# Optimization experiments

Hardware: AMD Instinct MI355X
Metric: run time of the kernel (lower is better)

## Reference

```python
import jax, jax.numpy as jnp
import numpy as np

B, S, DIM = 2, 2048, 4096
H, KVH = 32, 8
HD = DIM // H          # 128
N_REP = H // KVH       # 4
ROPE_THETA = 500000.0


def setup_inputs() -> dict:
    key = jax.random.key(0)
    ks = jax.random.split(key, 6)
    x = jax.random.normal(ks[0], (B, S, DIM), dtype=jnp.float32)
    sc = 1.0 / np.sqrt(DIM)
    wq = jax.random.normal(ks[1], (DIM, DIM), dtype=jnp.float32) * sc
    wk = jax.random.normal(ks[2], (KVH * HD, DIM), dtype=jnp.float32) * sc
    wv = jax.random.normal(ks[3], (KVH * HD, DIM), dtype=jnp.float32) * sc
    wo = jax.random.normal(ks[4], (DIM, DIM), dtype=jnp.float32) * sc
    # freqs_cis = exp(i * t * theta^{-2k/d}) -> cos/sin tables, shape (S, HD//2)
    inv_freq = 1.0 / (ROPE_THETA ** (np.arange(0, HD, 2, dtype=np.float32) / HD))
    t = np.arange(S, dtype=np.float32)
    angles = jnp.asarray(np.outer(t, inv_freq), dtype=jnp.float32)
    freqs_cos = jnp.cos(angles)
    freqs_sin = jnp.sin(angles)
    # causal additive mask (start_pos = 0 prefill)
    mask = jnp.triu(jnp.full((S, S), -1e9, dtype=jnp.float32), k=1)
    return {"x": x, "wq": wq, "wk": wk, "wv": wv, "wo": wo,
            "freqs_cos": freqs_cos, "freqs_sin": freqs_sin,
            "mask": mask, "start_pos": 0}


def _apply_rope(t, cos, sin):
    # t: [B,S,h,HD]; cos/sin: [S,HD//2] -> complex mult on pairs of last dim
    tr = t.reshape(*t.shape[:-1], HD // 2, 2)
    re, im = tr[..., 0], tr[..., 1]
    c = cos[None, :, None, :]
    s = sin[None, :, None, :]
    out_re = re * c - im * s
    out_im = re * s + im * c
    return jnp.stack([out_re, out_im], axis=-1).reshape(t.shape)


def reference(x, wq, wk, wv, wo, freqs_cos, freqs_sin, mask, start_pos):
    b, s, _ = x.shape
    xq = (x @ wq.T).reshape(b, s, H, HD)
    xk = (x @ wk.T).reshape(b, s, KVH, HD)
    xv = (x @ wv.T).reshape(b, s, KVH, HD)
    xq = _apply_rope(xq, freqs_cos, freqs_sin)
    xk = _apply_rope(xk, freqs_cos, freqs_sin)
    # start_pos == 0: KV cache slice [:, :start_pos+seqlen] == current xk/xv
    keys = jnp.repeat(xk, N_REP, axis=2)    # GQA expand -> [b,s,H,HD]
    values = jnp.repeat(xv, N_REP, axis=2)
    scores = jnp.einsum('bqhd,bkhd->bhqk', xq, keys) / jnp.sqrt(jnp.float32(HD))
    scores = scores + mask[None, None, :, :]
    probs = jax.nn.softmax(scores.astype(jnp.float32), axis=-1).astype(xq.dtype)
    out = jnp.einsum('bhqk,bkhd->bqhd', probs, values).reshape(b, s, H * HD)
    return out @ wo.T
```

## Files before the change

kernel.cpp:

```cpp
#include <hip/hip_runtime.h>


#define HN   32
#define KVHN 8
#define HDIM 128
#define SEQ  2048
#define NB   2
#define DIMM 4096
#define KVD  1024

typedef __attribute__((ext_vector_type(4))) float floatx4;
typedef __attribute__((ext_vector_type(8))) short bf16x8;
typedef unsigned short u16;
typedef unsigned int   u32;

__device__ __forceinline__ u16 f2bf(float f) {
  union { float f; u32 u; } x; x.f = f;
  u32 r = x.u + 0x7fffu + ((x.u >> 16) & 1u);
  return (u16)(r >> 16);
}

__device__ __forceinline__ void gload_lds16(const u16* g, u16* l) {
  __builtin_amdgcn_global_load_lds(
      (const __attribute__((address_space(1))) void*)g,
      (__attribute__((address_space(3))) void*)l, 16, 0, 0);
}

__global__ __launch_bounds__(256) void cast_f2bf_kernel(const float* __restrict__ in,
                                                        u16* __restrict__ out, int n) {
  int i = (blockIdx.x * 256 + threadIdx.x) * 8;
  if (i + 8 > n) return;
  const float4* p = (const float4*)(in + i);
  float4 a = p[0], b = p[1];
  union { u16 h[8]; uint4 v; } r;
  r.h[0] = f2bf(a.x); r.h[1] = f2bf(a.y); r.h[2] = f2bf(a.z); r.h[3] = f2bf(a.w);
  r.h[4] = f2bf(b.x); r.h[5] = f2bf(b.y); r.h[6] = f2bf(b.z); r.h[7] = f2bf(b.w);
  *(uint4*)(out + i) = r.v;
}


#define STG(tile, kind) do {                                                     \
    const int _t = (tile);                                                       \
    if (_t < NT) {                                                               \
      const int _kt = _t << 6;                                                   \
      u16* _buf = smem + ((_t & 1) << 15);                                       \
      const int _isB = (kind) & 1;                                               \
      const u16* _g = _isB ? Bb : Ab;                                            \
      u16* _lb = _isB ? _buf + 16384 : _buf;                                     \
      const int _hh = ((kind) >> 1);                                             \
      _Pragma("unroll")                                                          \
      for (int _cc = 0; _cc < 2; ++_cc) {                                        \
        const int _slot = _cc * 8 + w;                                           \
        const int _rb = _isB ? ((_slot >> 2) * 64 + _hh * 32 + (_slot & 3) * 8)  \
                             : ((_slot >> 3) * 128 + _hh * 64 + (_slot & 7) * 8);\
        const int _lrow = _rb + (l >> 3);                                        \
        const int _ck = (l & 7) ^ (l >> 3);                                      \
        gload_lds16(_g + (long)_lrow * K + _kt + _ck * 8,                        \
                    _lb + _rb * 64);                                             \
      }                                                                          \
    }                                                                            \
  } while (0)

#define LDA(bufAp, mh) do {                                                      \
    _Pragma("unroll") for (int mi = 0; mi < 4; ++mi)                             \
    _Pragma("unroll") for (int kk = 0; kk < 2; ++kk)                             \
      af[mi][kk] = *(const bf16x8*)&(bufAp)[                                     \
          (wm * 128 + (mh) * 64 + mi * 16 + c) * 64 + (((kk * 4 + g) ^ swz) * 8)]; \
  } while (0)

#define LDB(bufBp, nh) do {                                                      \
    _Pragma("unroll") for (int nj = 0; nj < 2; ++nj)                             \
    _Pragma("unroll") for (int kk = 0; kk < 2; ++kk)                             \
      bf[nh][nj][kk] = *(const bf16x8*)&(bufBp)[                                 \
          (wn * 64 + (nh) * 32 + nj * 16 + c) * 64 + (((kk * 4 + g) ^ swz) * 8)]; \
  } while (0)

#define MF16(mh, nh) do {                                                        \
    asm volatile("s_waitcnt lgkmcnt(0)");                                        \
    __builtin_amdgcn_s_setprio(1);                                               \
    _Pragma("unroll") for (int kk = 0; kk < 2; ++kk)                             \
    _Pragma("unroll") for (int mi = 0; mi < 4; ++mi)                             \
    _Pragma("unroll") for (int nj = 0; nj < 2; ++nj)                             \
      acc[mh][mi][nh][nj] = __builtin_amdgcn_mfma_f32_16x16x32_bf16(             \
          af[mi][kk], bf[nh][nj][kk], acc[mh][mi][nh][nj], 0, 0, 0);             \
    __builtin_amdgcn_s_setprio(0);                                               \
  } while (0)

#define BARF() do { asm volatile("" ::: "memory");                               \
                    __builtin_amdgcn_s_barrier();                                \
                    asm volatile("" ::: "memory"); } while (0)

#define HALF_ITER(curA, curB, s1t, s1k, s2t, s2k, s3t, s3k, s4t, s4k, LAST) do { \
    LDA(curA, 0); LDB(curB, 0); STG(s1t, s1k);                                   \
    BARF(); MF16(0, 0); BARF();                                                  \
    LDB(curB, 1); STG(s2t, s2k);                                                 \
    BARF(); MF16(0, 1); BARF();                                                  \
    LDA(curA, 1); STG(s3t, s3k);                                                 \
    BARF(); MF16(1, 0); BARF();                                                  \
    STG(s4t, s4k);                                                               \
    BARF(); MF16(1, 1);                                                          \
    if (LAST) { asm volatile("s_waitcnt vmcnt(0)" ::: "memory"); }               \
    else      { asm volatile("s_waitcnt vmcnt(6)" ::: "memory"); }               \
    BARF();                                                                      \
  } while (0)

template <int EPI>
__global__ __launch_bounds__(512, 2) void gemm256_nt(const u16* __restrict__ A, const u16* __restrict__ B,
                                                     void* __restrict__ Cv, void* __restrict__ Cv2,
                                                     int M, int N, int K,
                                                     const float* __restrict__ fc, const float* __restrict__ fs) {
  __shared__ u16 smem[65536];
  const int tid = threadIdx.x;
  const int w = tid >> 6, l = tid & 63, g = l >> 4, c = l & 15;
  const int wm = w >> 2, wn = w & 3;
  const int swz = c & 7;

  const int nwg = gridDim.x * gridDim.y;
  int lid = blockIdx.y * gridDim.x + blockIdx.x;
  lid = (lid & 7) * (nwg >> 3) + (lid >> 3);
  const int bx = lid % gridDim.x, by = lid / gridDim.x;
  const int m0 = by * 256, n0 = bx * 256;

  const u16* Ab = A + (long)m0 * K;
  const u16* Bb = B + (long)n0 * K;
  const int NT = K >> 6;
  const int NITER = NT >> 1;

  floatx4 acc[2][4][2][2] = {};
  bf16x8 af[4][2], bf[2][2][2];

  STG(0, 0); STG(0, 1); STG(0, 2); STG(0, 3);
  STG(1, 0); STG(1, 1); STG(1, 2);
  asm volatile("s_waitcnt vmcnt(6)" ::: "memory");
  BARF();

  const u16* A0p = smem;
  const u16* B0p = smem + 16384;
  const u16* A1p = smem + 32768;
  const u16* B1p = smem + 49152;

#pragma unroll 1
  for (int i = 0; i < NITER; ++i) {
    const bool last = (i == NITER - 1);
    const int t2 = 2 * i + 2, t3 = 2 * i + 3;
    HALF_ITER(A0p, B0p, 2 * i + 1, 3, t2, 0, t2, 1, t2, 2, last);
    HALF_ITER(A1p, B1p, t2, 3, t3, 0, t3, 1, t3, 2, last);
  }

#pragma unroll
  for (int mh = 0; mh < 2; ++mh)
#pragma unroll
  for (int mi = 0; mi < 4; ++mi)
#pragma unroll
  for (int nh = 0; nh < 2; ++nh)
#pragma unroll
  for (int nj = 0; nj < 2; ++nj) {
    const int colb = n0 + wn * 64 + nh * 32 + nj * 16;
    const int col = colb + c;
    const int rowb = m0 + wm * 128 + mh * 64 + mi * 16 + g * 4;
    floatx4 av = acc[mh][mi][nh][nj];
    if (EPI == 3 && colb >= 1024) {
      const int bb = rowb >> 11, s0 = rowb & (SEQ - 1);
      union { u16 h4[4]; uint2 v; } pk;
#pragma unroll
      for (int r = 0; r < 4; ++r) pk.h4[r] = f2bf(av[r]);
      *(uint2*)((u16*)Cv2 + ((long)(bb * 1024 + (col - 1024))) * SEQ + s0) = pk.v;
    } else {
#pragma unroll
      for (int r = 0; r < 4; ++r) {
        const int row = rowb + r;
        float v = av[r];
        if (EPI == 1 || EPI == 3) {
          float pv = __shfl_xor(v, 1);
          int pos = row & (SEQ - 1);
          int fi = (col & (HDIM - 1)) >> 1;
          float cs = fc[pos * (HDIM / 2) + fi];
          float sn = fs[pos * (HDIM / 2) + fi];
          v = (col & 1) ? (pv * sn + v * cs) : (v * cs - pv * sn);
          if (EPI == 1) v *= 0.08838834764831845f;
        }
        if (EPI == 2)      ((float*)Cv)[(long)row * N + col] = v;
        else if (EPI == 3) ((u16*)Cv)[(long)row * KVD + col] = f2bf(v);
        else               ((u16*)Cv)[(long)row * N + col] = f2bf(v);
      }
    }
  }
}

__global__ __launch_bounds__(256, 4) void flash_attn(const u16* __restrict__ q, const u16* __restrict__ kk,
                                                     const u16* __restrict__ vt, u16* __restrict__ o) {
  __shared__ u16 smem[20480];
  const int tid = threadIdx.x;
  const int w = tid >> 6, l = tid & 63, g = (l >> 4) & 3, c = l & 15;
  const int bh = blockIdx.y, b = bh >> 5, h = bh & 31, kvh = h >> 2;
  const int q0 = (31 - blockIdx.x) * 64;

  const u16* qg = q  + (long)(b * SEQ + q0) * DIMM + h * HDIM;
  const u16* kg = kk + (long)b * SEQ * KVD + kvh * HDIM;
  const u16* vg = vt + (long)(b * KVD + kvh * HDIM) * SEQ;

  const int r4 = l >> 4, ka16 = l & 15, r8 = l >> 3, ka8 = l & 7;

  {
#pragma unroll
    for (int cc = 0; cc < 4; ++cc) {
      int row = cc * 16 + w * 4 + r4;
      gload_lds16(qg + (long)row * DIMM + ((ka16 ^ (row & 7)) * 8), &smem[(cc * 16 + w * 4) * 128]);
    }
  }
  __syncthreads();
  bf16x8 qf[4];
#pragma unroll
  for (int t = 0; t < 4; ++t)
    qf[t] = *(const bf16x8*)&smem[(w * 16 + c) * 128 + ((t * 4 + g) ^ (c & 7)) * 8];
  __syncthreads();

  u16* sP = &smem[16384 + w * 1024];
  floatx4 oacc[8] = {};
  float mrow = -3e38f, lrow = 0.f;
  const int nkt = (q0 + 64) >> 6;
  const int qwave = q0 + w * 16;

#pragma unroll
  for (int cc = 0; cc < 4; ++cc) {
    int srow = cc * 16 + w * 4 + r4;
    gload_lds16(kg + (long)srow * KVD + ((ka16 ^ (srow & 7)) * 8), &smem[(cc * 16 + w * 4) * 128]);
  }
#pragma unroll
  for (int cc = 0; cc < 4; ++cc) {
    int drow = cc * 32 + w * 8 + r8;
    gload_lds16(vg + (long)drow * SEQ + ((ka8 ^ (drow & 7)) * 8), &smem[8192 + (cc * 32 + w * 8) * 64]);
  }
  __syncthreads();

  for (int j = 0; j < nkt; ++j) {
    floatx4 sc[4] = {};
#pragma unroll
    for (int ms = 0; ms < 4; ++ms) {
      bf16x8 kf[4];
#pragma unroll
      for (int t = 0; t < 4; ++t)
        kf[t] = *(const bf16x8*)&smem[(ms * 16 + c) * 128 + ((t * 4 + g) ^ (c & 7)) * 8];
#pragma unroll
      for (int t = 0; t < 4; ++t)
        sc[ms] = __builtin_amdgcn_mfma_f32_16x16x32_bf16(kf[t], qf[t], sc[ms], 0, 0, 0);
    }
    __syncthreads();

    if (j + 1 < nkt) {
#pragma unroll
      for (int cc = 0; cc < 4; ++cc) {
        int srow = cc * 16 + w * 4 + r4;
        gload_lds16(kg + (long)((j + 1) * 64 + srow) * KVD + ((ka16 ^ (srow & 7)) * 8),
                    &smem[(cc * 16 + w * 4) * 128]);
      }
    }

    {
      const bool needMask = (j * 64 + 63) > qwave;
      const int qv = qwave + c;
      float mx = -3e38f;
#pragma unroll
      for (int ms = 0; ms < 4; ++ms) {
        const int sbase = j * 64 + ms * 16 + g * 4;
#pragma unroll
        for (int r = 0; r < 4; ++r) {
          float v = sc[ms][r];
          if (needMask && (sbase + r > qv)) v = -1e9f;
          sc[ms][r] = v;
          mx = fmaxf(mx, v);
        }
      }
      mx = fmaxf(mx, __shfl_xor(mx, 16));
      mx = fmaxf(mx, __shfl_xor(mx, 32));
      const float mnew = fmaxf(mrow, mx);
      const float alpha = __expf(mrow - mnew);
      mrow = mnew;
      float rs = 0.f;
#pragma unroll
      for (int ms = 0; ms < 4; ++ms)
#pragma unroll
        for (int r = 0; r < 4; ++r) {
          float p = __expf(sc[ms][r] - mnew);
          sc[ms][r] = p;
          rs += p;
        }
      rs += __shfl_xor(rs, 16);
      rs += __shfl_xor(rs, 32);
      lrow = lrow * alpha + rs;
#pragma unroll
      for (int md = 0; md < 8; ++md) oacc[md] *= alpha;
#pragma unroll
      for (int ms = 0; ms < 4; ++ms) {
        u32 lo = (u32)f2bf(sc[ms][0]) | ((u32)f2bf(sc[ms][1]) << 16);
        u32 hi = (u32)f2bf(sc[ms][2]) | ((u32)f2bf(sc[ms][3]) << 16);
        uint2 val; val.x = lo; val.y = hi;
        const int sc16 = ms * 2 + (g >> 1);
        *(uint2*)&sP[c * 64 + ((sc16 ^ (c & 7)) * 8) + (g & 1) * 4] = val;
      }
    }

    bf16x8 pf[2];
#pragma unroll
    for (int kb2 = 0; kb2 < 2; ++kb2)
      pf[kb2] = *(const bf16x8*)&sP[c * 64 + (((kb2 * 4 + g) ^ (c & 7)) * 8)];
#pragma unroll
    for (int md = 0; md < 8; ++md)
#pragma unroll
      for (int kb2 = 0; kb2 < 2; ++kb2) {
        bf16x8 vf = *(const bf16x8*)&smem[8192 + (md * 16 + c) * 64 + (((kb2 * 4 + g) ^ (c & 7)) * 8)];
        oacc[md] = __builtin_amdgcn_mfma_f32_16x16x32_bf16(vf, pf[kb2], oacc[md], 0, 0, 0);
      }
    __syncthreads();

    if (j + 1 < nkt) {
#pragma unroll
      for (int cc = 0; cc < 4; ++cc) {
        int drow = cc * 32 + w * 8 + r8;
        gload_lds16(vg + (long)drow * SEQ + (j + 1) * 64 + ((ka8 ^ (drow & 7)) * 8),
                    &smem[8192 + (cc * 32 + w * 8) * 64]);
      }
    }
  }

  u16* ob = o + (long)(b * SEQ + q0 + w * 16) * DIMM + h * HDIM;
  const float inv = 1.f / lrow;
#pragma unroll
  for (int md = 0; md < 8; ++md) {
    union { u16 h4[4]; uint2 v; } pk;
#pragma unroll
    for (int r = 0; r < 4; ++r) pk.h4[r] = f2bf(oacc[md][r] * inv);
    *(uint2*)&ob[(long)c * DIMM + md * 16 + g * 4] = pk.v;
  }
}

extern "C" void kernel_launch(void* const* d_in, const int* in_sizes, int n_in,
                              void* d_out, int out_size, void* d_ws, size_t ws_size,
                              hipStream_t stream) {
  (void)in_sizes; (void)n_in; (void)out_size; (void)ws_size;
  const float* x  = (const float*)d_in[0];
  const float* wq = (const float*)d_in[1];
  const float* wk = (const float*)d_in[2];
  const float* wv = (const float*)d_in[3];
  const float* wo = (const float*)d_in[4];
  const float* fc = (const float*)d_in[5];
  const float* fs = (const float*)d_in[6];

  u16* xb  = (u16*)d_ws;
  u16* w16 = xb  + 16777216;
  u16* qb  = w16 + 16777216;
  u16* kb  = qb  + 16777216;
  u16* vT  = kb  + 4194304;
  u16* ab  = vT  + 4194304;

  const int M = NB * SEQ;

  cast_f2bf_kernel<<<16777216 / 2048, 256, 0, stream>>>(x,  xb,  16777216);
  cast_f2bf_kernel<<<16777216 / 2048, 256, 0, stream>>>(wq, w16, 16777216);
  gemm256_nt<1><<<dim3(16, 16), 512, 0, stream>>>(xb, w16, qb, nullptr, M, DIMM, DIMM, fc, fs);
  cast_f2bf_kernel<<<4194304 / 2048, 256, 0, stream>>>(wk, w16, 4194304);
  cast_f2bf_kernel<<<4194304 / 2048, 256, 0, stream>>>(wv, w16 + 4194304, 4194304);
  gemm256_nt<3><<<dim3(8, 16), 512, 0, stream>>>(xb, w16, kb, vT, M, 2048, DIMM, fc, fs);
  flash_attn<<<dim3(32, 64), 256, 0, stream>>>(qb, kb, vT, ab);
  cast_f2bf_kernel<<<16777216 / 2048, 256, 0, stream>>>(wo, w16, 16777216);
  gemm256_nt<2><<<dim3(16, 16), 512, 0, stream>>>(ab, w16, d_out, nullptr, M, DIMM, DIMM, nullptr, nullptr);
}
```

Measured before the change: 793.8 us.

## Double flash-attention query tile to 128 rows and switch softmax to exp2

```diff
diff --git a/kernel.cpp b/kernel.cpp
--- a/kernel.cpp
+++ b/kernel.cpp
@@ -18,6 +18,14 @@
   union { float f; u32 u; } x; x.f = f;
   u32 r = x.u + 0x7fffu + ((x.u >> 16) & 1u);
   return (u16)(r >> 16);
+}
+
+__device__ __forceinline__ float fexp2(float x) {
+#if __has_builtin(__builtin_amdgcn_exp2f)
+  return __builtin_amdgcn_exp2f(x);
+#else
+  return exp2f(x);
+#endif
 }
 
 __device__ __forceinline__ void gload_lds16(const u16* g, u16* l) {
@@ -177,7 +185,7 @@
           float cs = fc[pos * (HDIM / 2) + fi];
           float sn = fs[pos * (HDIM / 2) + fi];
           v = (col & 1) ? (pv * sn + v * cs) : (v * cs - pv * sn);
-          if (EPI == 1) v *= 0.08838834764831845f;
+          if (EPI == 1) v *= 0.12751744590279677f;
         }
         if (EPI == 2)      ((float*)Cv)[(long)row * N + col] = v;
         else if (EPI == 3) ((u16*)Cv)[(long)row * KVD + col] = f2bf(v);
@@ -187,13 +195,13 @@
   }
 }
 
-__global__ __launch_bounds__(256, 4) void flash_attn(const u16* __restrict__ q, const u16* __restrict__ kk,
-                                                     const u16* __restrict__ vt, u16* __restrict__ o) {
-  __shared__ u16 smem[20480];
+__global__ __launch_bounds__(256) void flash_attn(const u16* __restrict__ q, const u16* __restrict__ kk,
+                                                  const u16* __restrict__ vt, u16* __restrict__ o) {
+  __shared__ u16 smem[24576];
   const int tid = threadIdx.x;
   const int w = tid >> 6, l = tid & 63, g = (l >> 4) & 3, c = l & 15;
   const int bh = blockIdx.y, b = bh >> 5, h = bh & 31, kvh = h >> 2;
-  const int q0 = (31 - blockIdx.x) * 64;
+  const int q0 = (15 - blockIdx.x) * 128;
 
   const u16* qg = q  + (long)(b * SEQ + q0) * DIMM + h * HDIM;
   const u16* kg = kk + (long)b * SEQ * KVD + kvh * HDIM;
@@ -201,25 +209,18 @@
 
   const int r4 = l >> 4, ka16 = l & 15, r8 = l >> 3, ka8 = l & 7;
 
-  {
-#pragma unroll
-    for (int cc = 0; cc < 4; ++cc) {
-      int row = cc * 16 + w * 4 + r4;
-      gload_lds16(qg + (long)row * DIMM + ((ka16 ^ (row & 7)) * 8), &smem[(cc * 16 + w * 4) * 128]);
-    }
-  }
-  __syncthreads();
-  bf16x8 qf[4];
-#pragma unroll
-  for (int t = 0; t < 4; ++t)
-    qf[t] = *(const bf16x8*)&smem[(w * 16 + c) * 128 + ((t * 4 + g) ^ (c & 7)) * 8];
-  __syncthreads();
-
-  u16* sP = &smem[16384 + w * 1024];
-  floatx4 oacc[8] = {};
-  float mrow = -3e38f, lrow = 0.f;
-  const int nkt = (q0 + 64) >> 6;
-  const int qwave = q0 + w * 16;
+  bf16x8 qf[2][4];
+#pragma unroll
+  for (int sub = 0; sub < 2; ++sub)
+#pragma unroll
+    for (int t = 0; t < 4; ++t)
+      qf[sub][t] = *(const bf16x8*)(qg + (long)(w * 32 + sub * 16 + c) * DIMM + t * 32 + g * 8);
+
+  u16* sP = &smem[16384 + w * 2048];
+  floatx4 oacc[2][8] = {};
+  float mrow[2] = {-3e38f, -3e38f}, lrow[2] = {0.f, 0.f};
+  const int nkt = (q0 >> 6) + 2;
+  const int qw0 = q0 + w * 32;
 
 #pragma unroll
   for (int cc = 0; cc < 4; ++cc) {
@@ -234,7 +235,7 @@
   __syncthreads();
 
   for (int j = 0; j < nkt; ++j) {
-    floatx4 sc[4] = {};
+    floatx4 sc[2][4] = {};
 #pragma unroll
     for (int ms = 0; ms < 4; ++ms) {
       bf16x8 kf[4];
@@ -242,8 +243,10 @@
       for (int t = 0; t < 4; ++t)
         kf[t] = *(const bf16x8*)&smem[(ms * 16 + c) * 128 + ((t * 4 + g) ^ (c & 7)) * 8];
 #pragma unroll
-      for (int t = 0; t < 4; ++t)
-        sc[ms] = __builtin_amdgcn_mfma_f32_16x16x32_bf16(kf[t], qf[t], sc[ms], 0, 0, 0);
+      for (int t = 0; t < 4; ++t) {
+        sc[0][ms] = __builtin_amdgcn_mfma_f32_16x16x32_bf16(kf[t], qf[0][t], sc[0][ms], 0, 0, 0);
+        sc[1][ms] = __builtin_amdgcn_mfma_f32_16x16x32_bf16(kf[t], qf[1][t], sc[1][ms], 0, 0, 0);
+      }
     }
     __syncthreads();
 
@@ -256,60 +259,64 @@
       }
     }
 
-    {
-      const bool needMask = (j * 64 + 63) > qwave;
-      const int qv = qwave + c;
+#pragma unroll
+    for (int sub = 0; sub < 2; ++sub) {
+      const bool needMask = (j * 64 + 63) > (qw0 + sub * 16);
+      const int qv = qw0 + sub * 16 + c;
       float mx = -3e38f;
 #pragma unroll
       for (int ms = 0; ms < 4; ++ms) {
         const int sbase = j * 64 + ms * 16 + g * 4;
 #pragma unroll
         for (int r = 0; r < 4; ++r) {
-          float v = sc[ms][r];
+          float v = sc[sub][ms][r];
           if (needMask && (sbase + r > qv)) v = -1e9f;
-          sc[ms][r] = v;
+          sc[sub][ms][r] = v;
           mx = fmaxf(mx, v);
         }
       }
       mx = fmaxf(mx, __shfl_xor(mx, 16));
       mx = fmaxf(mx, __shfl_xor(mx, 32));
-      const float mnew = fmaxf(mrow, mx);
-      const float alpha = __expf(mrow - mnew);
-      mrow = mnew;
+      const float mnew = fmaxf(mrow[sub], mx);
+      const float alpha = fexp2(mrow[sub] - mnew);
+      mrow[sub] = mnew;
       float rs = 0.f;
 #pragma unroll
       for (int ms = 0; ms < 4; ++ms)
 #pragma unroll
         for (int r = 0; r < 4; ++r) {
-          float p = __expf(sc[ms][r] - mnew);
-          sc[ms][r] = p;
+          float p = fexp2(sc[sub][ms][r] - mnew);
+          sc[sub][ms][r] = p;
           rs += p;
         }
       rs += __shfl_xor(rs, 16);
       rs += __shfl_xor(rs, 32);
-      lrow = lrow * alpha + rs;
-#pragma unroll
-      for (int md = 0; md < 8; ++md) oacc[md] *= alpha;
+      lrow[sub] = lrow[sub] * alpha + rs;
+#pragma unroll
+      for (int md = 0; md < 8; ++md) oacc[sub][md] *= alpha;
 #pragma unroll
       for (int ms = 0; ms < 4; ++ms) {
-        u32 lo = (u32)f2bf(sc[ms][0]) | ((u32)f2bf(sc[ms][1]) << 16);
-        u32 hi = (u32)f2bf(sc[ms][2]) | ((u32)f2bf(sc[ms][3]) << 16);
+        u32 lo = (u32)f2bf(sc[sub][ms][0]) | ((u32)f2bf(sc[sub][ms][1]) << 16);
+        u32 hi = (u32)f2bf(sc[sub][ms][2]) | ((u32)f2bf(sc[sub][ms][3]) << 16);
         uint2 val; val.x = lo; val.y = hi;
         const int sc16 = ms * 2 + (g >> 1);
-        *(uint2*)&sP[c * 64 + ((sc16 ^ (c & 7)) * 8) + (g & 1) * 4] = val;
-      }
-    }
-
-    bf16x8 pf[2];
-#pragma unroll
-    for (int kb2 = 0; kb2 < 2; ++kb2)
-      pf[kb2] = *(const bf16x8*)&sP[c * 64 + (((kb2 * 4 + g) ^ (c & 7)) * 8)];
+        *(uint2*)&sP[(sub * 16 + c) * 64 + ((sc16 ^ (c & 7)) * 8) + (g & 1) * 4] = val;
+      }
+    }
+
+    bf16x8 pf[2][2];
+#pragma unroll
+    for (int sub = 0; sub < 2; ++sub)
+#pragma unroll
+      for (int kb2 = 0; kb2 < 2; ++kb2)
+        pf[sub][kb2] = *(const bf16x8*)&sP[(sub * 16 + c) * 64 + (((kb2 * 4 + g) ^ (c & 7)) * 8)];
 #pragma unroll
     for (int md = 0; md < 8; ++md)
 #pragma unroll
       for (int kb2 = 0; kb2 < 2; ++kb2) {
         bf16x8 vf = *(const bf16x8*)&smem[8192 + (md * 16 + c) * 64 + (((kb2 * 4 + g) ^ (c & 7)) * 8)];
-        oacc[md] = __builtin_amdgcn_mfma_f32_16x16x32_bf16(vf, pf[kb2], oacc[md], 0, 0, 0);
+        oacc[0][md] = __builtin_amdgcn_mfma_f32_16x16x32_bf16(vf, pf[0][kb2], oacc[0][md], 0, 0, 0);
+        oacc[1][md] = __builtin_amdgcn_mfma_f32_16x16x32_bf16(vf, pf[1][kb2], oacc[1][md], 0, 0, 0);
       }
     __syncthreads();
 
@@ -323,14 +330,17 @@
     }
   }
 
-  u16* ob = o + (long)(b * SEQ + q0 + w * 16) * DIMM + h * HDIM;
-  const float inv = 1.f / lrow;
-#pragma unroll
-  for (int md = 0; md < 8; ++md) {
-    union { u16 h4[4]; uint2 v; } pk;
-#pragma unroll
-    for (int r = 0; r < 4; ++r) pk.h4[r] = f2bf(oacc[md][r] * inv);
-    *(uint2*)&ob[(long)c * DIMM + md * 16 + g * 4] = pk.v;
+#pragma unroll
+  for (int sub = 0; sub < 2; ++sub) {
+    u16* ob = o + (long)(b * SEQ + q0 + w * 32 + sub * 16) * DIMM + h * HDIM;
+    const float inv = 1.f / lrow[sub];
+#pragma unroll
+    for (int md = 0; md < 8; ++md) {
+      union { u16 h4[4]; uint2 v; } pk;
+#pragma unroll
+      for (int r = 0; r < 4; ++r) pk.h4[r] = f2bf(oacc[sub][md][r] * inv);
+      *(uint2*)&ob[(long)c * DIMM + md * 16 + g * 4] = pk.v;
+    }
   }
 }
 
@@ -361,7 +371,7 @@
   cast_f2bf_kernel<<<4194304 / 2048, 256, 0, stream>>>(wk, w16, 4194304);
   cast_f2bf_kernel<<<4194304 / 2048, 256, 0, stream>>>(wv, w16 + 4194304, 4194304);
   gemm256_nt<3><<<dim3(8, 16), 512, 0, stream>>>(xb, w16, kb, vT, M, 2048, DIMM, fc, fs);
-  flash_attn<<<dim3(32, 64), 256, 0, stream>>>(qb, kb, vT, ab);
+  flash_attn<<<dim3(16, 64), 256, 0, stream>>>(qb, kb, vT, ab);
   cast_f2bf_kernel<<<16777216 / 2048, 256, 0, stream>>>(wo, w16, 16777216);
   gemm256_nt<2><<<dim3(16, 16), 512, 0, stream>>>(ab, w16, d_out, nullptr, M, DIMM, DIMM, nullptr, nullptr);
 }
```

Result: slower. 898.4 us (+13.2%).

## Pair causal query tiles per block and use exp2 with packed bf16 conversion

Applied to the files above, without the earlier changes.

```diff
diff --git a/kernel.cpp b/kernel.cpp
--- a/kernel.cpp
+++ b/kernel.cpp
@@ -18,6 +18,20 @@
   union { float f; u32 u; } x; x.f = f;
   u32 r = x.u + 0x7fffu + ((x.u >> 16) & 1u);
   return (u16)(r >> 16);
+}
+
+__device__ __forceinline__ u32 cvtpk_bf16(float a, float b) {
+  u32 r;
+  asm("v_cvt_pk_bf16_f32 %0, %1, %2" : "=v"(r) : "v"(a), "v"(b));
+  return r;
+}
+
+__device__ __forceinline__ float fexp2(float x) {
+#if __has_builtin(__builtin_amdgcn_exp2f)
+  return __builtin_amdgcn_exp2f(x);
+#else
+  return exp2f(x);
+#endif
 }
 
 __device__ __forceinline__ void gload_lds16(const u16* g, u16* l) {
@@ -177,7 +191,7 @@
           float cs = fc[pos * (HDIM / 2) + fi];
           float sn = fs[pos * (HDIM / 2) + fi];
           v = (col & 1) ? (pv * sn + v * cs) : (v * cs - pv * sn);
-          if (EPI == 1) v *= 0.08838834764831845f;
+          if (EPI == 1) v *= 0.12751744590279677f;
         }
         if (EPI == 2)      ((float*)Cv)[(long)row * N + col] = v;
         else if (EPI == 3) ((u16*)Cv)[(long)row * KVD + col] = f2bf(v);
@@ -187,150 +201,145 @@
   }
 }
 
-__global__ __launch_bounds__(256, 4) void flash_attn(const u16* __restrict__ q, const u16* __restrict__ kk,
-                                                     const u16* __restrict__ vt, u16* __restrict__ o) {
+__global__ __launch_bounds__(256) void flash_attn(const u16* __restrict__ q, const u16* __restrict__ kk,
+                                                  const u16* __restrict__ vt, u16* __restrict__ o) {
   __shared__ u16 smem[20480];
   const int tid = threadIdx.x;
   const int w = tid >> 6, l = tid & 63, g = (l >> 4) & 3, c = l & 15;
   const int bh = blockIdx.y, b = bh >> 5, h = bh & 31, kvh = h >> 2;
-  const int q0 = (31 - blockIdx.x) * 64;
-
-  const u16* qg = q  + (long)(b * SEQ + q0) * DIMM + h * HDIM;
+  const int r4 = l >> 4, ka16 = l & 15, r8 = l >> 3, ka8 = l & 7;
+
   const u16* kg = kk + (long)b * SEQ * KVD + kvh * HDIM;
   const u16* vg = vt + (long)(b * KVD + kvh * HDIM) * SEQ;
-
-  const int r4 = l >> 4, ka16 = l & 15, r8 = l >> 3, ka8 = l & 7;
-
-  {
+  u16* sP = &smem[16384 + w * 1024];
+
+#pragma unroll 1
+  for (int pass = 0; pass < 2; ++pass) {
+    const int qblk = pass ? (int)blockIdx.x : 31 - (int)blockIdx.x;
+    const int q0 = qblk * 64;
+    const u16* qg = q + (long)(b * SEQ + q0) * DIMM + h * HDIM;
+
+    bf16x8 qf[4];
+#pragma unroll
+    for (int t = 0; t < 4; ++t)
+      qf[t] = *(const bf16x8*)(qg + (long)(w * 16 + c) * DIMM + t * 32 + g * 8);
+
+    floatx4 oacc[8] = {};
+    float mrow = -3e38f, lrow = 0.f;
+    const int nkt = qblk + 1;
+    const int qwave = q0 + w * 16;
+
 #pragma unroll
     for (int cc = 0; cc < 4; ++cc) {
-      int row = cc * 16 + w * 4 + r4;
-      gload_lds16(qg + (long)row * DIMM + ((ka16 ^ (row & 7)) * 8), &smem[(cc * 16 + w * 4) * 128]);
-    }
-  }
-  __syncthreads();
-  bf16x8 qf[4];
-#pragma unroll
-  for (int t = 0; t < 4; ++t)
-    qf[t] = *(const bf16x8*)&smem[(w * 16 + c) * 128 + ((t * 4 + g) ^ (c & 7)) * 8];
-  __syncthreads();
-
-  u16* sP = &smem[16384 + w * 1024];
-  floatx4 oacc[8] = {};
-  float mrow = -3e38f, lrow = 0.f;
-  const int nkt = (q0 + 64) >> 6;
-  const int qwave = q0 + w * 16;
-
-#pragma unroll
-  for (int cc = 0; cc < 4; ++cc) {
-    int srow = cc * 16 + w * 4 + r4;
-    gload_lds16(kg + (long)srow * KVD + ((ka16 ^ (srow & 7)) * 8), &smem[(cc * 16 + w * 4) * 128]);
-  }
-#pragma unroll
-  for (int cc = 0; cc < 4; ++cc) {
-    int drow = cc * 32 + w * 8 + r8;
-    gload_lds16(vg + (long)drow * SEQ + ((ka8 ^ (drow & 7)) * 8), &smem[8192 + (cc * 32 + w * 8) * 64]);
-  }
-  __syncthreads();
-
-  for (int j = 0; j < nkt; ++j) {
-    floatx4 sc[4] = {};
-#pragma unroll
-    for (int ms = 0; ms < 4; ++ms) {
-      bf16x8 kf[4];
-#pragma unroll
-      for (int t = 0; t < 4; ++t)
-        kf[t] = *(const bf16x8*)&smem[(ms * 16 + c) * 128 + ((t * 4 + g) ^ (c & 7)) * 8];
-#pragma unroll
-      for (int t = 0; t < 4; ++t)
-        sc[ms] = __builtin_amdgcn_mfma_f32_16x16x32_bf16(kf[t], qf[t], sc[ms], 0, 0, 0);
+      int srow = cc * 16 + w * 4 + r4;
+      gload_lds16(kg + (long)srow * KVD + ((ka16 ^ (srow & 7)) * 8), &smem[(cc * 16 + w * 4) * 128]);
+    }
+#pragma unroll
+    for (int cc = 0; cc < 4; ++cc) {
+      int drow = cc * 32 + w * 8 + r8;
+      gload_lds16(vg + (long)drow * SEQ + ((ka8 ^ (drow & 7)) * 8), &smem[8192 + (cc * 32 + w * 8) * 64]);
     }
     __syncthreads();
 
-    if (j + 1 < nkt) {
-#pragma unroll
-      for (int cc = 0; cc < 4; ++cc) {
-        int srow = cc * 16 + w * 4 + r4;
-        gload_lds16(kg + (long)((j + 1) * 64 + srow) * KVD + ((ka16 ^ (srow & 7)) * 8),
-                    &smem[(cc * 16 + w * 4) * 128]);
-      }
-    }
-
-    {
-      const bool needMask = (j * 64 + 63) > qwave;
-      const int qv = qwave + c;
-      float mx = -3e38f;
+    for (int j = 0; j < nkt; ++j) {
+      floatx4 sc[4] = {};
 #pragma unroll
       for (int ms = 0; ms < 4; ++ms) {
-        const int sbase = j * 64 + ms * 16 + g * 4;
-#pragma unroll
-        for (int r = 0; r < 4; ++r) {
-          float v = sc[ms][r];
-          if (needMask && (sbase + r > qv)) v = -1e9f;
-          sc[ms][r] = v;
-          mx = fmaxf(mx, v);
-        }
-      }
-      mx = fmaxf(mx, __shfl_xor(mx, 16));
-      mx = fmaxf(mx, __shfl_xor(mx, 32));
-      const float mnew = fmaxf(mrow, mx);
-      const float alpha = __expf(mrow - mnew);
-      mrow = mnew;
-      float rs = 0.f;
-#pragma unroll
-      for (int ms = 0; ms < 4; ++ms)
-#pragma unroll
-        for (int r = 0; r < 4; ++r) {
-          float p = __expf(sc[ms][r] - mnew);
-          sc[ms][r] = p;
-          rs += p;
-        }
-      rs += __shfl_xor(rs, 16);
-      rs += __shfl_xor(rs, 32);
-      lrow = lrow * alpha + rs;
-#pragma unroll
-      for (int md = 0; md < 8; ++md) oacc[md] *= alpha;
-#pragma unroll
-      for (int ms = 0; ms < 4; ++ms) {
-        u32 lo = (u32)f2bf(sc[ms][0]) | ((u32)f2bf(sc[ms][1]) << 16);
-        u32 hi = (u32)f2bf(sc[ms][2]) | ((u32)f2bf(sc[ms][3]) << 16);
-        uint2 val; val.x = lo; val.y = hi;
-        const int sc16 = ms * 2 + (g >> 1);
-        *(uint2*)&sP[c * 64 + ((sc16 ^ (c & 7)) * 8) + (g & 1) * 4] = val;
-      }
-    }
-
-    bf16x8 pf[2];
-#pragma unroll
-    for (int kb2 = 0; kb2 < 2; ++kb2)
-      pf[kb2] = *(const bf16x8*)&sP[c * 64 + (((kb2 * 4 + g) ^ (c & 7)) * 8)];
-#pragma unroll
-    for (int md = 0; md < 8; ++md)
-#pragma unroll
-      for (int kb2 = 0; kb2 < 2; ++kb2) {
-        bf16x8 vf = *(const bf16x8*)&smem[8192 + (md * 16 + c) * 64 + (((kb2 * 4 + g) ^ (c & 7)) * 8)];
-        oacc[md] = __builtin_amdgcn_mfma_f32_16x16x32_bf16(vf, pf[kb2], oacc[md], 0, 0, 0);
-      }
-    __syncthreads();
-
-    if (j + 1 < nkt) {
-#pragma unroll
-      for (int cc = 0; cc < 4; ++cc) {
-        int drow = cc * 32 + w * 8 + r8;
-        gload_lds16(vg + (long)drow * SEQ + (j + 1) * 64 + ((ka8 ^ (drow & 7)) * 8),
-                    &smem[8192 + (cc * 32 + w * 8) * 64]);
-      }
-    }
-  }
-
-  u16* ob = o + (long)(b * SEQ + q0 + w * 16) * DIMM + h * HDIM;
-  const float inv = 1.f / lrow;
-#pragma unroll
-  for (int md = 0; md < 8; ++md) {
-    union { u16 h4[4]; uint2 v; } pk;
-#pragma unroll
-    for (int r = 0; r < 4; ++r) pk.h4[r] = f2bf(oacc[md][r] * inv);
-    *(uint2*)&ob[(long)c * DIMM + md * 16 + g * 4] = pk.v;
+        bf16x8 kf[4];
+#pragma unroll
+        for (int t = 0; t < 4; ++t)
+          kf[t] = *(const bf16x8*)&smem[(ms * 16 + c) * 128 + ((t * 4 + g) ^ (c & 7)) * 8];
+#pragma unroll
+        for (int t = 0; t < 4; ++t)
+          sc[ms] = __builtin_amdgcn_mfma_f32_16x16x32_bf16(kf[t], qf[t], sc[ms], 0, 0, 0);
+      }
+      __syncthreads();
+
+      if (j + 1 < nkt) {
+#pragma unroll
+        for (int cc = 0; cc < 4; ++cc) {
+          int srow = cc * 16 + w * 4 + r4;
+          gload_lds16(kg + (long)((j + 1) * 64 + srow) * KVD + ((ka16 ^ (srow & 7)) * 8),
+                      &smem[(cc * 16 + w * 4) * 128]);
+        }
+      }
+
+      {
+        const bool needMask = (j * 64 + 63) > qwave;
+        const int qv = qwave + c;
+        float mx = -3e38f;
+#pragma unroll
+        for (int ms = 0; ms < 4; ++ms) {
+          const int sbase = j * 64 + ms * 16 + g * 4;
+#pragma unroll
+          for (int r = 0; r < 4; ++r) {
+            float v = sc[ms][r];
+            if (needMask && (sbase + r > qv)) v = -1e9f;
+            sc[ms][r] = v;
+            mx = fmaxf(mx, v);
+          }
+        }
+        mx = fmaxf(mx, __shfl_xor(mx, 16));
+        mx = fmaxf(mx, __shfl_xor(mx, 32));
+        const float mnew = fmaxf(mrow, mx);
+        const float alpha = fexp2(mrow - mnew);
+        mrow = mnew;
+        float rs = 0.f;
+#pragma unroll
+        for (int ms = 0; ms < 4; ++ms)
+#pragma unroll
+          for (int r = 0; r < 4; ++r) {
+            float p = fexp2(sc[ms][r] - mnew);
+            sc[ms][r] = p;
+            rs += p;
+          }
+        rs += __shfl_xor(rs, 16);
+        rs += __shfl_xor(rs, 32);
+        lrow = lrow * alpha + rs;
+#pragma unroll
+        for (int md = 0; md < 8; ++md) oacc[md] *= alpha;
+#pragma unroll
+        for (int ms = 0; ms < 4; ++ms) {
+          uint2 val;
+          val.x = cvtpk_bf16(sc[ms][0], sc[ms][1]);
+          val.y = cvtpk_bf16(sc[ms][2], sc[ms][3]);
+          const int sc16 = ms * 2 + (g >> 1);
+          *(uint2*)&sP[c * 64 + ((sc16 ^ (c & 7)) * 8) + (g & 1) * 4] = val;
+        }
+      }
+
+      bf16x8 pf[2];
+#pragma unroll
+      for (int kb2 = 0; kb2 < 2; ++kb2)
+        pf[kb2] = *(const bf16x8*)&sP[c * 64 + (((kb2 * 4 + g) ^ (c & 7)) * 8)];
+#pragma unroll
+      for (int md = 0; md < 8; ++md)
+#pragma unroll
+        for (int kb2 = 0; kb2 < 2; ++kb2) {
+          bf16x8 vf = *(const bf16x8*)&smem[8192 + (md * 16 + c) * 64 + (((kb2 * 4 + g) ^ (c & 7)) * 8)];
+          oacc[md] = __builtin_amdgcn_mfma_f32_16x16x32_bf16(vf, pf[kb2], oacc[md], 0, 0, 0);
+        }
+      __syncthreads();
+
+      if (j + 1 < nkt) {
+#pragma unroll
+        for (int cc = 0; cc < 4; ++cc) {
+          int drow = cc * 32 + w * 8 + r8;
+          gload_lds16(vg + (long)drow * SEQ + (j + 1) * 64 + ((ka8 ^ (drow & 7)) * 8),
+                      &smem[8192 + (cc * 32 + w * 8) * 64]);
+        }
+      }
+    }
+
+    u16* ob = o + (long)(b * SEQ + q0 + w * 16) * DIMM + h * HDIM;
+    const float inv = 1.f / lrow;
+#pragma unroll
+    for (int md = 0; md < 8; ++md) {
+      uint2 pk;
+      pk.x = cvtpk_bf16(oacc[md][0] * inv, oacc[md][1] * inv);
+      pk.y = cvtpk_bf16(oacc[md][2] * inv, oacc[md][3] * inv);
+      *(uint2*)&ob[(long)c * DIMM + md * 16 + g * 4] = pk;
+    }
   }
 }
 
@@ -361,7 +370,7 @@
   cast_f2bf_kernel<<<4194304 / 2048, 256, 0, stream>>>(wk, w16, 4194304);
   cast_f2bf_kernel<<<4194304 / 2048, 256, 0, stream>>>(wv, w16 + 4194304, 4194304);
   gemm256_nt<3><<<dim3(8, 16), 512, 0, stream>>>(xb, w16, kb, vT, M, 2048, DIMM, fc, fs);
-  flash_attn<<<dim3(32, 64), 256, 0, stream>>>(qb, kb, vT, ab);
+  flash_attn<<<dim3(16, 64), 256, 0, stream>>>(qb, kb, vT, ab);
   cast_f2bf_kernel<<<16777216 / 2048, 256, 0, stream>>>(wo, w16, 16777216);
   gemm256_nt<2><<<dim3(16, 16), 512, 0, stream>>>(ab, w16, d_out, nullptr, M, DIMM, DIMM, nullptr, nullptr);
 }
```

Result: faster. 718.7 us (-9.5%).
